# Performance work log

Hardware: AMD Instinct MI355X
Metric: run time of the kernel (lower is better)

## Reference

```python
import jax, jax.numpy as jnp
import numpy as np

B, T, M, P = 2048, 64, 256, 256


def setup_inputs() -> dict:
    key = jax.random.key(0)
    ks = jax.random.split(key, 16)
    s = 0.05
    return {
        "encoded_inputs": jax.random.normal(ks[0], (B, T, M), jnp.float32),
        "y": jax.random.normal(ks[1], (B, T, 1), jnp.float32),
        # W_d: Linear(2P -> M)
        "W_d_w": jax.random.normal(ks[2], (M, 2 * P), jnp.float32) * s,
        "W_d_b": jax.random.normal(ks[3], (M,), jnp.float32) * s,
        # U_d: Linear(M -> M, no bias)
        "U_d_w": jax.random.normal(ks[4], (M, M), jnp.float32) * s,
        # v_d: Linear(M -> 1, no bias)
        "v_d_w": jax.random.normal(ks[5], (1, M), jnp.float32) * s,
        # w_tilda: Linear(M+1 -> 1)
        "w_tilda_w": jax.random.normal(ks[6], (1, M + 1), jnp.float32) * s,
        "w_tilda_b": jax.random.normal(ks[7], (1,), jnp.float32) * s,
        # W_y: Linear(P+M -> P)
        "W_y_w": jax.random.normal(ks[8], (P, P + M), jnp.float32) * s,
        "W_y_b": jax.random.normal(ks[9], (P,), jnp.float32) * s,
        # v_y: Linear(P -> 1)
        "v_y_w": jax.random.normal(ks[10], (1, P), jnp.float32) * s,
        "v_y_b": jax.random.normal(ks[11], (1,), jnp.float32) * s,
        # LSTMCell(input=1, hidden=P): gate order i, f, g, o
        "W_ih": jax.random.normal(ks[12], (4 * P, 1), jnp.float32) * s,
        "W_hh": jax.random.normal(ks[13], (4 * P, P), jnp.float32) * s,
        "b_ih": jax.random.normal(ks[14], (4 * P,), jnp.float32) * s,
        "b_hh": jax.random.normal(ks[15], (4 * P,), jnp.float32) * s,
    }


def _forward(encoded_inputs, y, W_d_w, W_d_b, U_d_w, v_d_w, w_tilda_w, w_tilda_b,
             W_y_w, W_y_b, v_y_w, v_y_b, W_ih, W_hh, b_ih, b_hh):
    b, T_enc, m = encoded_inputs.shape
    p = W_hh.shape[1]
    T_steps = y.shape[1]

    # U_d(encoded_inputs) is time-step invariant: precompute once. [B, T_enc, M]
    Ue = jnp.einsum("btm,nm->btn", encoded_inputs, U_d_w)

    def lstm_cell(x, h, c):
        gates = x @ W_ih.T + b_ih + h @ W_hh.T + b_hh  # [B, 4P]
        i, f, g, o = jnp.split(gates, 4, axis=1)
        c_new = jax.nn.sigmoid(f) * c + jax.nn.sigmoid(i) * jnp.tanh(g)
        h_new = jax.nn.sigmoid(o) * jnp.tanh(c_new)
        return h_new, c_new

    def step(carry, y_t):
        d, s_prime, _, _ = carry
        ds = jnp.concatenate([d, s_prime], axis=1)           # [B, 2P]
        x1 = ds @ W_d_w.T + W_d_b                            # [B, M]
        z1 = jnp.tanh(x1[:, None, :] + Ue)                   # [B, T_enc, M]
        l_t = jnp.einsum("btm,m->bt", z1, v_d_w[0])          # [B, T_enc]
        beta = jax.nn.softmax(l_t, axis=1)                   # [B, T_enc]
        c_t = jnp.einsum("bt,btm->bm", beta, encoded_inputs) # [B, M]
        yc = jnp.concatenate([c_t, y_t], axis=1)             # [B, M+1]
        y_tilda = yc @ w_tilda_w.T + w_tilda_b               # [B, 1]
        d_new, s_new = lstm_cell(y_tilda, d, s_prime)
        return (d_new, s_new, c_t, beta), None

    init = (
        jnp.zeros((b, p), encoded_inputs.dtype),
        jnp.zeros((b, p), encoded_inputs.dtype),
        jnp.zeros((b, m), encoded_inputs.dtype),
        jnp.zeros((b, T_enc), encoded_inputs.dtype),
    )
    y_seq = jnp.transpose(y, (1, 0, 2))  # [T, B, 1]
    (d, s_prime, c_t, beta), _ = jax.lax.scan(step, init, y_seq)

    dc = jnp.concatenate([d, c_t], axis=1)                   # [B, P+M]
    y_Tp1 = (dc @ W_y_w.T + W_y_b) @ v_y_w.T + v_y_b         # [B, 1]
    return y_Tp1, beta[:, :, None]


def reference(encoded_inputs, y, W_d_w, W_d_b, U_d_w, v_d_w, w_tilda_w, w_tilda_b,
              W_y_w, W_y_b, v_y_w, v_y_b, W_ih, W_hh, b_ih, b_hh):
    return _forward(encoded_inputs, y, W_d_w, W_d_b, U_d_w, v_d_w, w_tilda_w,
                    w_tilda_b, W_y_w, W_y_b, v_y_w, v_y_b, W_ih, W_hh, b_ih, b_hh)
```

## Files before the change

kernel.cpp:

```cpp
#include <hip/hip_runtime.h>
#include <math.h>

#define BB 2048
#define TT 64
#define MM 256

typedef __attribute__((ext_vector_type(8))) unsigned short u16x8;

__device__ __forceinline__ float bf2f(unsigned short u) {
    union { unsigned int i; float f; } v; v.i = ((unsigned int)u) << 16; return v.f;
}
__device__ __forceinline__ unsigned short f2bf(float f) {
    union { float f; unsigned int i; } v; v.f = f;
    const unsigned int r = v.i + 0x7fff + ((v.i >> 16) & 1);
    return (unsigned short)(r >> 16);
}

#if __has_builtin(__builtin_amdgcn_exp2f)
#define EXP2F(x) __builtin_amdgcn_exp2f(x)
#else
#define EXP2F(x) __expf((x) * 0.6931471805599453f)
#endif
#if __has_builtin(__builtin_amdgcn_rcpf)
#define RCPF(x) __builtin_amdgcn_rcpf(x)
#else
#define RCPF(x) (1.0f / (x))
#endif

#define TSC 2.885390081777927f

__global__ __launch_bounds__(256) void gemm64_bf(
    const float* __restrict__ A, int lda,
    const float* __restrict__ W, int ldw,
    unsigned short* __restrict__ C, int ldc, int K)
{
    __shared__ float As[64][36];
    __shared__ float Ws[64][36];

    const int tid = threadIdx.x;
    const int row0 = blockIdx.x * 64;
    const int col0 = blockIdx.y * 64;

    const int lr = tid >> 3;
    const int lc4 = (tid & 7) * 4;
    const int tx = tid & 15;
    const int ty = tid >> 4;

    float acc[4][4] = {{0.f}};

    for (int k0 = 0; k0 < K; k0 += 32) {
        const float4 a0 = *(const float4*)&A[(size_t)(row0 + lr) * lda + k0 + lc4];
        const float4 a1 = *(const float4*)&A[(size_t)(row0 + lr + 32) * lda + k0 + lc4];
        const float4 w0 = *(const float4*)&W[(size_t)(col0 + lr) * ldw + k0 + lc4];
        const float4 w1 = *(const float4*)&W[(size_t)(col0 + lr + 32) * ldw + k0 + lc4];
        *(float4*)&As[lr][lc4] = a0;
        *(float4*)&As[lr + 32][lc4] = a1;
        *(float4*)&Ws[lr][lc4] = w0;
        *(float4*)&Ws[lr + 32][lc4] = w1;
        __syncthreads();

        #pragma unroll
        for (int kk = 0; kk < 32; kk += 4) {
            float4 a[4], w[4];
            #pragma unroll
            for (int i = 0; i < 4; i++) a[i] = *(const float4*)&As[ty + 16 * i][kk];
            #pragma unroll
            for (int j = 0; j < 4; j++) w[j] = *(const float4*)&Ws[tx + 16 * j][kk];
            #pragma unroll
            for (int i = 0; i < 4; i++)
                #pragma unroll
                for (int j = 0; j < 4; j++) {
                    acc[i][j] += a[i].x * w[j].x;
                    acc[i][j] += a[i].y * w[j].y;
                    acc[i][j] += a[i].z * w[j].z;
                    acc[i][j] += a[i].w * w[j].w;
                }
        }
        __syncthreads();
    }

    #pragma unroll
    for (int i = 0; i < 4; i++) {
        const int rr = row0 + ty + 16 * i;
        #pragma unroll
        for (int j = 0; j < 4; j++)
            C[(size_t)rr * ldc + col0 + tx + 16 * j] = f2bf(acc[i][j]);
    }
}

__global__ __launch_bounds__(512) void compute_q(
    const float* __restrict__ enc, const float* __restrict__ w_t_w,
    float* __restrict__ q)
{
    const int row = blockIdx.x * 8 + (threadIdx.x >> 6);
    const int lane = threadIdx.x & 63;
    const float4 e = *(const float4*)&enc[(size_t)row * MM + lane * 4];
    const float4 w = *(const float4*)&w_t_w[lane * 4];
    float s = e.x * w.x + e.y * w.y + e.z * w.z + e.w * w.w;
    #pragma unroll
    for (int off = 32; off > 0; off >>= 1) s += __shfl_down(s, off);
    if (lane == 0) q[row] = s;
}

__global__ __launch_bounds__(512) void fused_decoder(
    const unsigned short* __restrict__ Ue,
    const float* __restrict__ enc,
    const float* __restrict__ y,
    const float* __restrict__ q,
    const float* __restrict__ W_d_w, const float* __restrict__ W_d_b,
    const float* __restrict__ v_d,
    const float* __restrict__ w_t_w, const float* __restrict__ w_t_b,
    const float* __restrict__ W_ih, const float* __restrict__ W_hh,
    const float* __restrict__ b_ih, const float* __restrict__ b_hh,
    const float* __restrict__ W_y_w, const float* __restrict__ W_y_b,
    const float* __restrict__ v_y_w, const float* __restrict__ v_y_b,
    float* __restrict__ out)
{
    const int tid = threadIdx.x;
    const int b0 = blockIdx.x * 8;
    const int r_a = tid >> 6;
    const int t_a = tid & 63;

    __shared__ __align__(16) float hc[8][512];
    __shared__ float gates[8][1024];
    __shared__ __align__(16) float2 xv[8][256];
    __shared__ float betas[8][64];
    __shared__ float ytl[8];
    __shared__ __align__(16) float ctx[8][256];
    __shared__ float wihs[1024];
    __shared__ float bsums[1024];
    __shared__ float red[4][8];
    __shared__ float vsum_s;

    float vdn = 0.f, bd = 0.f;
    if (tid < 256) {
        vdn = v_d[tid];
        bd = W_d_b[tid];
        #pragma unroll
        for (int r = 0; r < 8; r++) {
            xv[r][tid] = make_float2(bd * TSC, vdn);
            hc[r][tid] = 0.f;
            hc[r][256 + tid] = 0.f;
        }
    }
    for (int i = tid; i < 1024; i += 512) {
        wihs[i] = W_ih[i];
        bsums[i] = b_ih[i] + b_hh[i];
    }
    for (int i = tid; i < 8 * 1024; i += 512) ((float*)gates)[i] = 0.f;

    if (tid < 64) {
        float s = v_d[tid] + v_d[tid + 64] + v_d[tid + 128] + v_d[tid + 192];
        #pragma unroll
        for (int off = 32; off > 0; off >>= 1) s += __shfl_down(s, off);
        if (tid == 0) vsum_s = s;
    }

    const float qreg = q[(size_t)(b0 + r_a) * TT + t_a];
    const float yreg = y[(size_t)(b0 + r_a) * TT + t_a];
    const float wty = w_t_w[256];
    const float wtb = w_t_b[0];

    __syncthreads();
    const float VS = vsum_s;

    const u16x8* __restrict__ uptr =
        (const u16x8*)(Ue + ((size_t)(b0 + r_a) * TT + t_a) * MM);

    for (int t = 0; t < TT; t++) {
        float acc = 0.f;
        {
            u16x8 u0 = uptr[0], u1 = uptr[1], u2 = uptr[2], u3 = uptr[3];
            #pragma unroll
            for (int blk = 0; blk < 8; blk++) {
                u16x8 n0, n1, n2, n3;
                if (blk < 7) {
                    n0 = uptr[blk * 4 + 4]; n1 = uptr[blk * 4 + 5];
                    n2 = uptr[blk * 4 + 6]; n3 = uptr[blk * 4 + 7];
                }
                const int mb = blk * 32;
                #define PROC8(uu, mm)                                              \
                    _Pragma("unroll")                                              \
                    for (int j = 0; j < 8; j += 2) {                               \
                        const float4 x2 = *(const float4*)&xv[r_a][(mm) + j];      \
                        const float a0 = fmaf(bf2f(uu[j]),     TSC, x2.x);         \
                        const float a1 = fmaf(bf2f(uu[j + 1]), TSC, x2.z);         \
                        acc = fmaf(x2.y, RCPF(EXP2F(a0) + 1.f), acc);              \
                        acc = fmaf(x2.w, RCPF(EXP2F(a1) + 1.f), acc);              \
                    }
                PROC8(u0, mb)
                PROC8(u1, mb + 8)
                PROC8(u2, mb + 16)
                PROC8(u3, mb + 24)
                #undef PROC8
                u0 = n0; u1 = n1; u2 = n2; u3 = n3;
            }
        }
        const float l = VS - 2.f * acc;

        float mx = l;
        #pragma unroll
        for (int off = 32; off > 0; off >>= 1) mx = fmaxf(mx, __shfl_xor(mx, off));
        const float e = __expf(l - mx);
        float sm = e;
        #pragma unroll
        for (int off = 32; off > 0; off >>= 1) sm += __shfl_xor(sm, off);
        const float bta = e * RCPF(sm);

        if (t == TT - 1) {
            betas[r_a][t_a] = bta;
            out[BB + (size_t)(b0 + r_a) * TT + t_a] = bta;
        }

        float part = bta * qreg;
        if (t_a == t) part += fmaf(wty, yreg, wtb);
        #pragma unroll
        for (int off = 32; off > 0; off >>= 1) part += __shfl_down(part, off);
        if (t_a == 0) ytl[r_a] = part;
        __syncthreads();

        {
            const int p = tid & 255;
            const int half = tid >> 8;
            #pragma unroll
            for (int j = 0; j < 4; j++) {
                const int r = half * 4 + j;
                const float x = ytl[r];
                const float gi = gates[r][p]       + x * wihs[p]       + bsums[p];
                const float gf = gates[r][p + 256] + x * wihs[p + 256] + bsums[p + 256];
                const float gg = gates[r][p + 512] + x * wihs[p + 512] + bsums[p + 512];
                const float go = gates[r][p + 768] + x * wihs[p + 768] + bsums[p + 768];
                const float c_old = hc[r][256 + p];
                const float si = RCPF(1.f + __expf(-gi));
                const float sf = RCPF(1.f + __expf(-gf));
                const float so = RCPF(1.f + __expf(-go));
                const float eg = __expf(2.f * gg);
                const float tg = 1.f - 2.f * RCPF(eg + 1.f);
                const float cn = sf * c_old + si * tg;
                const float ec = __expf(2.f * cn);
                const float tc = 1.f - 2.f * RCPF(ec + 1.f);
                hc[r][p] = so * tc;
                hc[r][256 + p] = cn;
            }
        }
        __syncthreads();

        if (t < TT - 1) {
            if (tid < 256) {
                const int n = tid;
                const float* __restrict__ wr = W_d_w + (size_t)n * 512;
                const float* __restrict__ wg = W_hh + (size_t)n * 256;
                float ax[8] = {0.f, 0.f, 0.f, 0.f, 0.f, 0.f, 0.f, 0.f};
                float ag[8] = {0.f, 0.f, 0.f, 0.f, 0.f, 0.f, 0.f, 0.f};
                #pragma unroll 2
                for (int k = 0; k < 256; k += 4) {
                    const float4 w1 = *(const float4*)(wr + k);
                    const float4 w2 = *(const float4*)(wr + 256 + k);
                    const float4 w3 = *(const float4*)(wg + k);
                    #pragma unroll
                    for (int r = 0; r < 8; r++) {
                        const float4 h4 = *(const float4*)&hc[r][k];
                        const float4 c4 = *(const float4*)&hc[r][256 + k];
                        ax[r] += w1.x * h4.x + w1.y * h4.y + w1.z * h4.z + w1.w * h4.w
                               + w2.x * c4.x + w2.y * c4.y + w2.z * c4.z + w2.w * c4.w;
                        ag[r] += w3.x * h4.x + w3.y * h4.y + w3.z * h4.z + w3.w * h4.w;
                    }
                }
                #pragma unroll
                for (int r = 0; r < 8; r++) {
                    xv[r][n] = make_float2((ax[r] + bd) * TSC, vdn);
                    gates[r][n] = ag[r];
                }
            } else {
                const int n2 = tid - 256;
                const float* __restrict__ wA = W_hh + (size_t)(n2 + 256) * 256;
                const float* __restrict__ wB = W_hh + (size_t)(n2 + 512) * 256;
                const float* __restrict__ wC = W_hh + (size_t)(n2 + 768) * 256;
                float aA[8] = {0.f, 0.f, 0.f, 0.f, 0.f, 0.f, 0.f, 0.f};
                float aB[8] = {0.f, 0.f, 0.f, 0.f, 0.f, 0.f, 0.f, 0.f};
                float aC[8] = {0.f, 0.f, 0.f, 0.f, 0.f, 0.f, 0.f, 0.f};
                #pragma unroll 2
                for (int k = 0; k < 256; k += 4) {
                    const float4 qa = *(const float4*)(wA + k);
                    const float4 qb = *(const float4*)(wB + k);
                    const float4 qc = *(const float4*)(wC + k);
                    #pragma unroll
                    for (int r = 0; r < 8; r++) {
                        const float4 h4 = *(const float4*)&hc[r][k];
                        aA[r] += qa.x * h4.x + qa.y * h4.y + qa.z * h4.z + qa.w * h4.w;
                        aB[r] += qb.x * h4.x + qb.y * h4.y + qb.z * h4.z + qb.w * h4.w;
                        aC[r] += qc.x * h4.x + qc.y * h4.y + qc.z * h4.z + qc.w * h4.w;
                    }
                }
                #pragma unroll
                for (int r = 0; r < 8; r++) {
                    gates[r][n2 + 256] = aA[r];
                    gates[r][n2 + 512] = aB[r];
                    gates[r][n2 + 768] = aC[r];
                }
            }
        }
        __syncthreads();
    }

    {
        const float* __restrict__ ep =
            enc + (size_t)(b0 + r_a) * TT * MM + t_a * 4;
        float c0 = 0.f, c1 = 0.f, c2 = 0.f, c3 = 0.f;
        #pragma unroll 4
        for (int tt2 = 0; tt2 < TT; tt2++) {
            const float4 e4 = *(const float4*)(ep + (size_t)tt2 * MM);
            const float bta = betas[r_a][tt2];
            c0 = fmaf(bta, e4.x, c0);
            c1 = fmaf(bta, e4.y, c1);
            c2 = fmaf(bta, e4.z, c2);
            c3 = fmaf(bta, e4.w, c3);
        }
        ctx[r_a][t_a * 4]     = c0;
        ctx[r_a][t_a * 4 + 1] = c1;
        ctx[r_a][t_a * 4 + 2] = c2;
        ctx[r_a][t_a * 4 + 3] = c3;
    }
    __syncthreads();

    if (tid < 256) {
        const int n = tid;
        const float* __restrict__ wr = W_y_w + (size_t)n * 512;
        float acc[8] = {0.f, 0.f, 0.f, 0.f, 0.f, 0.f, 0.f, 0.f};
        #pragma unroll 2
        for (int k = 0; k < 256; k += 4) {
            const float4 wh = *(const float4*)(wr + k);
            const float4 wc = *(const float4*)(wr + 256 + k);
            #pragma unroll
            for (int r = 0; r < 8; r++) {
                const float4 h4 = *(const float4*)&hc[r][k];
                const float4 c4 = *(const float4*)&ctx[r][k];
                acc[r] += wh.x * h4.x + wh.y * h4.y + wh.z * h4.z + wh.w * h4.w
                        + wc.x * c4.x + wc.y * c4.y + wc.z * c4.z + wc.w * c4.w;
            }
        }
        const float vy = v_y_w[n];
        const float by = W_y_b[n];
        const int wv = tid >> 6;
        const int lane = tid & 63;
        #pragma unroll
        for (int r = 0; r < 8; r++) {
            float v = (acc[r] + by) * vy;
            #pragma unroll
            for (int off = 32; off > 0; off >>= 1) v += __shfl_down(v, off);
            if (lane == 0) red[wv][r] = v;
        }
    }
    __syncthreads();
    if (tid < 8)
        out[b0 + tid] = red[0][tid] + red[1][tid] + red[2][tid] + red[3][tid] + v_y_b[0];
}

extern "C" void kernel_launch(void* const* d_in, const int* in_sizes, int n_in,
                              void* d_out, int out_size, void* d_ws, size_t ws_size,
                              hipStream_t stream)
{
    const float* enc      = (const float*)d_in[0];
    const float* y        = (const float*)d_in[1];
    const float* W_d_w    = (const float*)d_in[2];
    const float* W_d_b    = (const float*)d_in[3];
    const float* U_d_w    = (const float*)d_in[4];
    const float* v_d_w    = (const float*)d_in[5];
    const float* w_tilda_w= (const float*)d_in[6];
    const float* w_tilda_b= (const float*)d_in[7];
    const float* W_y_w    = (const float*)d_in[8];
    const float* W_y_b    = (const float*)d_in[9];
    const float* v_y_w    = (const float*)d_in[10];
    const float* v_y_b    = (const float*)d_in[11];
    const float* W_ih     = (const float*)d_in[12];
    const float* W_hh     = (const float*)d_in[13];
    const float* b_ih     = (const float*)d_in[14];
    const float* b_hh     = (const float*)d_in[15];

    float* out = (float*)d_out;

    unsigned short* Ue_bf = (unsigned short*)d_ws;
    float* qbuf = (float*)(Ue_bf + (size_t)BB * TT * MM);

    gemm64_bf<<<dim3(BB * TT / 64, MM / 64), 256, 0, stream>>>(
        enc, MM, U_d_w, MM, Ue_bf, MM, MM);

    compute_q<<<BB * TT / 8, 512, 0, stream>>>(enc, w_tilda_w, qbuf);

    fused_decoder<<<BB / 8, 512, 0, stream>>>(
        Ue_bf, enc, y, qbuf, W_d_w, W_d_b, v_d_w, w_tilda_w, w_tilda_b,
        W_ih, W_hh, b_ih, b_hh, W_y_w, W_y_b, v_y_w, v_y_b, out);
}
```

Baseline: 5.400 ms.

## Double decoder block to 1024 threads, splitting attention over M halves

The fused decoder now launches 1024 threads per block. Two wavefronts share each batch row and each handles half of the M dimension in the attention tanh-sum, with the partial sums combined through shared memory and an extra barrier. The recurrent W_hh gate matvec is spread so each thread computes one gate row, and the W_d matvec uses register prefetch of weights. The aim is to raise parallelism and shorten the per-step serial critical path, at the cost of an additional __syncthreads per step and higher register pressure under the 1024-thread launch bound.

```diff
diff --git a/kernel.cpp b/kernel.cpp
--- a/kernel.cpp
+++ b/kernel.cpp
@@ -102,7 +102,7 @@
     if (lane == 0) q[row] = s;
 }
 
-__global__ __launch_bounds__(512) void fused_decoder(
+__global__ __launch_bounds__(1024, 4) void fused_decoder(
     const unsigned short* __restrict__ Ue,
     const float* __restrict__ enc,
     const float* __restrict__ y,
@@ -118,12 +118,16 @@
 {
     const int tid = threadIdx.x;
     const int b0 = blockIdx.x * 8;
-    const int r_a = tid >> 6;
-    const int t_a = tid & 63;
+    const int wv = tid >> 6;
+    const int lane = tid & 63;
+    const int r_a = wv >> 1;
+    const int mh  = wv & 1;
+    const int t_a = lane;
 
     __shared__ __align__(16) float hc[8][512];
     __shared__ float gates[8][1024];
     __shared__ __align__(16) float2 xv[8][256];
+    __shared__ float lpart[8][2][64];
     __shared__ float betas[8][64];
     __shared__ float ytl[8];
     __shared__ __align__(16) float ctx[8][256];
@@ -137,17 +141,15 @@
         vdn = v_d[tid];
         bd = W_d_b[tid];
         #pragma unroll
-        for (int r = 0; r < 8; r++) {
+        for (int r = 0; r < 8; r++)
             xv[r][tid] = make_float2(bd * TSC, vdn);
-            hc[r][tid] = 0.f;
-            hc[r][256 + tid] = 0.f;
-        }
-    }
-    for (int i = tid; i < 1024; i += 512) {
-        wihs[i] = W_ih[i];
-        bsums[i] = b_ih[i] + b_hh[i];
-    }
-    for (int i = tid; i < 8 * 1024; i += 512) ((float*)gates)[i] = 0.f;
+    }
+    wihs[tid & 1023] = W_ih[tid & 1023];
+    bsums[tid & 1023] = b_ih[tid & 1023] + b_hh[tid & 1023];
+    #pragma unroll
+    for (int i = 0; i < 8; i++) ((float*)gates)[tid + i * 1024] = 0.f;
+    #pragma unroll
+    for (int i = 0; i < 4; i++) ((float*)hc)[tid + i * 1024] = 0.f;
 
     if (tid < 64) {
         float s = v_d[tid] + v_d[tid + 64] + v_d[tid + 128] + v_d[tid + 192];
@@ -165,20 +167,21 @@
     const float VS = vsum_s;
 
     const u16x8* __restrict__ uptr =
-        (const u16x8*)(Ue + ((size_t)(b0 + r_a) * TT + t_a) * MM);
+        (const u16x8*)(Ue + ((size_t)(b0 + r_a) * TT + t_a) * MM + mh * 128);
+    const int mbase = mh * 128;
 
     for (int t = 0; t < TT; t++) {
         float acc = 0.f;
         {
             u16x8 u0 = uptr[0], u1 = uptr[1], u2 = uptr[2], u3 = uptr[3];
             #pragma unroll
-            for (int blk = 0; blk < 8; blk++) {
+            for (int blk = 0; blk < 4; blk++) {
                 u16x8 n0, n1, n2, n3;
-                if (blk < 7) {
+                if (blk < 3) {
                     n0 = uptr[blk * 4 + 4]; n1 = uptr[blk * 4 + 5];
                     n2 = uptr[blk * 4 + 6]; n3 = uptr[blk * 4 + 7];
                 }
-                const int mb = blk * 32;
+                const int mb = mbase + blk * 32;
                 #define PROC8(uu, mm)                                              \
                     _Pragma("unroll")                                              \
                     for (int j = 0; j < 8; j += 2) {                               \
@@ -196,8 +199,10 @@
                 u0 = n0; u1 = n1; u2 = n2; u3 = n3;
             }
         }
-        const float l = VS - 2.f * acc;
-
+        lpart[r_a][mh][t_a] = acc;
+        __syncthreads();
+
+        const float l = VS - 2.f * (lpart[r_a][0][t_a] + lpart[r_a][1][t_a]);
         float mx = l;
         #pragma unroll
         for (int off = 32; off > 0; off >>= 1) mx = fmaxf(mx, __shfl_xor(mx, off));
@@ -207,24 +212,25 @@
         for (int off = 32; off > 0; off >>= 1) sm += __shfl_xor(sm, off);
         const float bta = e * RCPF(sm);
 
-        if (t == TT - 1) {
-            betas[r_a][t_a] = bta;
-            out[BB + (size_t)(b0 + r_a) * TT + t_a] = bta;
-        }
-
-        float part = bta * qreg;
-        if (t_a == t) part += fmaf(wty, yreg, wtb);
-        #pragma unroll
-        for (int off = 32; off > 0; off >>= 1) part += __shfl_down(part, off);
-        if (t_a == 0) ytl[r_a] = part;
+        if (mh == 0) {
+            if (t == TT - 1) {
+                betas[r_a][t_a] = bta;
+                out[BB + (size_t)(b0 + r_a) * TT + t_a] = bta;
+            }
+            float part = bta * qreg;
+            if (t_a == t) part += fmaf(wty, yreg, wtb);
+            #pragma unroll
+            for (int off = 32; off > 0; off >>= 1) part += __shfl_down(part, off);
+            if (t_a == 0) ytl[r_a] = part;
+        }
         __syncthreads();
 
         {
             const int p = tid & 255;
-            const int half = tid >> 8;
-            #pragma unroll
-            for (int j = 0; j < 4; j++) {
-                const int r = half * 4 + j;
+            const int rb2 = (tid >> 8) * 2;
+            #pragma unroll
+            for (int j = 0; j < 2; j++) {
+                const int r = rb2 + j;
                 const float x = ytl[r];
                 const float gi = gates[r][p]       + x * wihs[p]       + bsums[p];
                 const float gf = gates[r][p + 256] + x * wihs[p + 256] + bsums[p + 256];
@@ -246,80 +252,67 @@
         __syncthreads();
 
         if (t < TT - 1) {
+            {
+                const int g = tid;
+                const float* __restrict__ wg = W_hh + (size_t)g * 256;
+                float ag[8] = {0.f, 0.f, 0.f, 0.f, 0.f, 0.f, 0.f, 0.f};
+                float4 w3 = *(const float4*)(wg);
+                for (int k = 0; k < 256; k += 4) {
+                    float4 nw3;
+                    if (k < 252) nw3 = *(const float4*)(wg + k + 4);
+                    #pragma unroll
+                    for (int r = 0; r < 8; r++) {
+                        const float4 h4 = *(const float4*)&hc[r][k];
+                        ag[r] += w3.x * h4.x + w3.y * h4.y + w3.z * h4.z + w3.w * h4.w;
+                    }
+                    w3 = nw3;
+                }
+                #pragma unroll
+                for (int r = 0; r < 8; r++) gates[r][g] = ag[r];
+            }
             if (tid < 256) {
                 const int n = tid;
                 const float* __restrict__ wr = W_d_w + (size_t)n * 512;
-                const float* __restrict__ wg = W_hh + (size_t)n * 256;
                 float ax[8] = {0.f, 0.f, 0.f, 0.f, 0.f, 0.f, 0.f, 0.f};
-                float ag[8] = {0.f, 0.f, 0.f, 0.f, 0.f, 0.f, 0.f, 0.f};
-                #pragma unroll 2
+                float4 w1 = *(const float4*)(wr);
+                float4 w2 = *(const float4*)(wr + 256);
                 for (int k = 0; k < 256; k += 4) {
-                    const float4 w1 = *(const float4*)(wr + k);
-                    const float4 w2 = *(const float4*)(wr + 256 + k);
-                    const float4 w3 = *(const float4*)(wg + k);
+                    float4 nw1, nw2;
+                    if (k < 252) {
+                        nw1 = *(const float4*)(wr + k + 4);
+                        nw2 = *(const float4*)(wr + 256 + k + 4);
+                    }
                     #pragma unroll
                     for (int r = 0; r < 8; r++) {
                         const float4 h4 = *(const float4*)&hc[r][k];
                         const float4 c4 = *(const float4*)&hc[r][256 + k];
                         ax[r] += w1.x * h4.x + w1.y * h4.y + w1.z * h4.z + w1.w * h4.w
                                + w2.x * c4.x + w2.y * c4.y + w2.z * c4.z + w2.w * c4.w;
-                        ag[r] += w3.x * h4.x + w3.y * h4.y + w3.z * h4.z + w3.w * h4.w;
                     }
+                    w1 = nw1; w2 = nw2;
                 }
                 #pragma unroll
-                for (int r = 0; r < 8; r++) {
+                for (int r = 0; r < 8; r++)
                     xv[r][n] = make_float2((ax[r] + bd) * TSC, vdn);
-                    gates[r][n] = ag[r];
-                }
-            } else {
-                const int n2 = tid - 256;
-                const float* __restrict__ wA = W_hh + (size_t)(n2 + 256) * 256;
-                const float* __restrict__ wB = W_hh + (size_t)(n2 + 512) * 256;
-                const float* __restrict__ wC = W_hh + (size_t)(n2 + 768) * 256;
-                float aA[8] = {0.f, 0.f, 0.f, 0.f, 0.f, 0.f, 0.f, 0.f};
-                float aB[8] = {0.f, 0.f, 0.f, 0.f, 0.f, 0.f, 0.f, 0.f};
-                float aC[8] = {0.f, 0.f, 0.f, 0.f, 0.f, 0.f, 0.f, 0.f};
-                #pragma unroll 2
-                for (int k = 0; k < 256; k += 4) {
-                    const float4 qa = *(const float4*)(wA + k);
-                    const float4 qb = *(const float4*)(wB + k);
-                    const float4 qc = *(const float4*)(wC + k);
-                    #pragma unroll
-                    for (int r = 0; r < 8; r++) {
-                        const float4 h4 = *(const float4*)&hc[r][k];
-                        aA[r] += qa.x * h4.x + qa.y * h4.y + qa.z * h4.z + qa.w * h4.w;
-                        aB[r] += qb.x * h4.x + qb.y * h4.y + qb.z * h4.z + qb.w * h4.w;
-                        aC[r] += qc.x * h4.x + qc.y * h4.y + qc.z * h4.z + qc.w * h4.w;
-                    }
-                }
-                #pragma unroll
-                for (int r = 0; r < 8; r++) {
-                    gates[r][n2 + 256] = aA[r];
-                    gates[r][n2 + 512] = aB[r];
-                    gates[r][n2 + 768] = aC[r];
-                }
             }
         }
         __syncthreads();
     }
 
     {
-        const float* __restrict__ ep =
-            enc + (size_t)(b0 + r_a) * TT * MM + t_a * 4;
-        float c0 = 0.f, c1 = 0.f, c2 = 0.f, c3 = 0.f;
-        #pragma unroll 4
+        const int r = tid >> 7;
+        const int m0 = (tid & 127) * 2;
+        const float* __restrict__ ep = enc + (size_t)(b0 + r) * TT * MM + m0;
+        float c0 = 0.f, c1 = 0.f;
+        #pragma unroll 8
         for (int tt2 = 0; tt2 < TT; tt2++) {
-            const float4 e4 = *(const float4*)(ep + (size_t)tt2 * MM);
-            const float bta = betas[r_a][tt2];
-            c0 = fmaf(bta, e4.x, c0);
-            c1 = fmaf(bta, e4.y, c1);
-            c2 = fmaf(bta, e4.z, c2);
-            c3 = fmaf(bta, e4.w, c3);
-        }
-        ctx[r_a][t_a * 4]     = c0;
-        ctx[r_a][t_a * 4 + 1] = c1;
-        ctx[r_a][t_a * 4 + 2] = c2;
-        ctx[r_a][t_a * 4 + 3] = c3;
+            const float2 e2 = *(const float2*)(ep + (size_t)tt2 * MM);
+            const float bta = betas[r][tt2];
+            c0 = fmaf(bta, e2.x, c0);
+            c1 = fmaf(bta, e2.y, c1);
+        }
+        ctx[r][m0] = c0;
+        ctx[r][m0 + 1] = c1;
     }
     __syncthreads();
 
@@ -341,14 +334,14 @@
         }
         const float vy = v_y_w[n];
         const float by = W_y_b[n];
-        const int wv = tid >> 6;
-        const int lane = tid & 63;
+        const int wv4 = tid >> 6;
+        const int ln = tid & 63;
         #pragma unroll
         for (int r = 0; r < 8; r++) {
             float v = (acc[r] + by) * vy;
             #pragma unroll
             for (int off = 32; off > 0; off >>= 1) v += __shfl_down(v, off);
-            if (lane == 0) red[wv][r] = v;
+            if (ln == 0) red[wv4][r] = v;
         }
     }
     __syncthreads();
@@ -387,7 +380,7 @@
 
     compute_q<<<BB * TT / 8, 512, 0, stream>>>(enc, w_tilda_w, qbuf);
 
-    fused_decoder<<<BB / 8, 512, 0, stream>>>(
+    fused_decoder<<<BB / 8, 1024, 0, stream>>>(
         Ue_bf, enc, y, qbuf, W_d_w, W_d_b, v_d_w, w_tilda_w, w_tilda_b,
         W_ih, W_hh, b_ih, b_hh, W_y_w, W_y_b, v_y_w, v_y_b, out);
 }
```

Result: slower. 9.568 ms (+77.2%).
